# Performance work log

Measured on AMD Instinct MI355X. Metric: run time of the kernel, lower is better.

## Reference

```python
import jax, jax.numpy as jnp
import numpy as np


def _hfreq_mask(c, scale):
    # zeros over the centered (shifted) low-frequency band, ones elsewhere
    m = np.ones((c,), dtype=np.complex64)
    m[c // 2 - c // scale: c // 2 + c // scale] = 0
    return jnp.asarray(m).reshape(1, 1, 1, c)


def setup_inputs() -> dict:
    key = jax.random.key(0)
    x = jax.random.normal(key, (32, 38, 38, 728), dtype=jnp.float32)
    return {"x": x, "scale": 4}


def reference(x, scale):
    c = x.shape[-1]
    norm = jnp.asarray(np.sqrt(c), dtype=jnp.complex64)
    X = jnp.fft.fft(x.astype(jnp.complex64), axis=-1) / norm
    X = jnp.fft.fftshift(X, axes=-1)
    X = X * _hfreq_mask(c, scale)
    X = jnp.fft.ifftshift(X, axes=-1)
    y = jnp.fft.ifft(X, axis=-1) * norm
    y = jnp.real(y).astype(jnp.float32)
    return jax.nn.relu(y)
```

## Files before the change

### kernel.cpp

```cpp
#include <hip/hip_runtime.h>
#include <hip/hip_bf16.h>

#define CC 728
#define KB 736
#define NPAD 768
#define M_ROWS 46208
#define KT 23
#define NWG 2166

typedef __attribute__((ext_vector_type(8))) short bf16x8;
typedef __attribute__((ext_vector_type(8))) unsigned short ushort8;
typedef __attribute__((ext_vector_type(4))) float f32x4;

__device__ __forceinline__ unsigned short f2bf(float f) {
    unsigned int u = __float_as_uint(f);
    unsigned int r = u + 0x7fffu + ((u >> 16) & 1u);
    return (unsigned short)(r >> 16);
}

__device__ __forceinline__ void gload_lds16(const void* g, void* l) {
    __builtin_amdgcn_global_load_lds(
        (const __attribute__((address_space(1))) void*)g,
        (__attribute__((address_space(3))) void*)l,
        16, 0, 0);
}

__global__ void build_bt(unsigned short* __restrict__ bt) {
    int idx = blockIdx.x * blockDim.x + threadIdx.x;
    if (idx >= NPAD * KB) return;
    int n = idx / KB, k = idx % KB;
    float v = 0.f;
    if (n < CC && k < CC) {
        int d = n - k; if (d < 0) d += CC;
        if (d == 0) v = 0.5f;
        else if (d & 1) {
            float t = (float)(3.14159265358979323846 * (double)d / (double)CC);
            float s = ((d >> 1) & 1) ? 1.f : -1.f;
            v = s * cosf(t) / ((float)CC * sinf(t));
        }
    }
    bt[idx] = f2bf(v);
}

__global__ __launch_bounds__(256) void gemm_relu(
        const float* __restrict__ x,
        const unsigned short* __restrict__ bt,
        float* __restrict__ out) {
    __shared__ unsigned short ldsA[128 * 32];
    __shared__ unsigned short ldsB[128 * 32];

    const int tid  = threadIdx.x;
    const int lane = tid & 63;
    const int wid  = tid >> 6;
    const int wr   = wid >> 1, wc = wid & 1;
    const int l15  = lane & 15, lhi = lane >> 4;

    const int NX = 8;
    int orig  = blockIdx.x;
    int q = NWG / NX, r = NWG % NX;
    int xcd = orig % NX, local = orig / NX;
    int wgid = (xcd < r ? xcd * (q + 1) : r * (q + 1) + (xcd - r) * q) + local;
    const int bm = (wgid / 6) * 128;
    const int bn = (wgid % 6) * 128;

    f32x4 acc[4][4];
#pragma unroll
    for (int i = 0; i < 4; ++i)
#pragma unroll
        for (int j = 0; j < 4; ++j)
#pragma unroll
            for (int rr = 0; rr < 4; ++rr) acc[i][j][rr] = 0.f;

    const int arow = tid >> 2;
    const int ac   = tid & 3;

    for (int kt = 0; kt < KT; ++kt) {
        const int k0 = kt * 32;

#pragma unroll
        for (int i = 0; i < 2; ++i) {
            int rr   = i * 64 + arow;
            int gsrc = (ac - (rr >> 1)) & 3;
            gload_lds16(bt + (size_t)(bn + rr) * KB + k0 + gsrc * 8,
                        &ldsB[(i * 256 + tid) * 8]);
        }

        float4 va0[2], va1[2];
        const bool full = (k0 + 32 <= CC);
#pragma unroll
        for (int i = 0; i < 2; ++i) {
            const float* src = x + (size_t)(bm + i * 64 + arow) * CC + k0 + ac * 8;
            if (full) {
                va0[i] = ((const float4*)src)[0];
                va1[i] = ((const float4*)src)[1];
            } else {
                int cb = k0 + ac * 8;
                va0[i] = (cb     < CC) ? ((const float4*)src)[0] : make_float4(0.f,0.f,0.f,0.f);
                va1[i] = (cb + 4 < CC) ? ((const float4*)src)[1] : make_float4(0.f,0.f,0.f,0.f);
            }
        }

#pragma unroll
        for (int i = 0; i < 2; ++i) {
            int rr = i * 64 + arow;
            int sc = (ac + (rr >> 1)) & 3;
            ushort8 o;
            o[0] = f2bf(va0[i].x); o[1] = f2bf(va0[i].y);
            o[2] = f2bf(va0[i].z); o[3] = f2bf(va0[i].w);
            o[4] = f2bf(va1[i].x); o[5] = f2bf(va1[i].y);
            o[6] = f2bf(va1[i].z); o[7] = f2bf(va1[i].w);
            *(ushort8*)&ldsA[(rr * 4 + sc) * 8] = o;
        }
        __syncthreads();

        bf16x8 a[4], b[4];
#pragma unroll
        for (int mi = 0; mi < 4; ++mi) {
            int row = wr * 64 + mi * 16 + l15;
            int c   = (lhi + (row >> 1)) & 3;
            a[mi] = *(const bf16x8*)&ldsA[(row * 4 + c) * 8];
        }
#pragma unroll
        for (int nj = 0; nj < 4; ++nj) {
            int row = wc * 64 + nj * 16 + l15;
            int c   = (lhi + (row >> 1)) & 3;
            b[nj] = *(const bf16x8*)&ldsB[(row * 4 + c) * 8];
        }
#pragma unroll
        for (int mi = 0; mi < 4; ++mi)
#pragma unroll
            for (int nj = 0; nj < 4; ++nj)
                acc[mi][nj] = __builtin_amdgcn_mfma_f32_16x16x32_bf16(
                    a[mi], b[nj], acc[mi][nj], 0, 0, 0);
        __syncthreads();
    }

#pragma unroll
    for (int mi = 0; mi < 4; ++mi) {
#pragma unroll
        for (int nj = 0; nj < 4; ++nj) {
            int colg = bn + wc * 64 + nj * 16 + l15;
            if (colg < CC) {
#pragma unroll
                for (int rr = 0; rr < 4; ++rr) {
                    int rowg = bm + wr * 64 + mi * 16 + lhi * 4 + rr;
                    float v = acc[mi][nj][rr];
                    out[(size_t)rowg * CC + colg] = v > 0.f ? v : 0.f;
                }
            }
        }
    }
}

extern "C" void kernel_launch(void* const* d_in, const int* in_sizes, int n_in,
                              void* d_out, int out_size, void* d_ws, size_t ws_size,
                              hipStream_t stream) {
    const float* x = (const float*)d_in[0];
    float* out = (float*)d_out;

    unsigned short* bt = (unsigned short*)d_ws;

    build_bt<<<(NPAD * KB + 255) / 256, 256, 0, stream>>>(bt);
    gemm_relu<<<NWG, 256, 0, stream>>>(x, bt, out);
}
```

Measured before the change: 118.7 us.

## Exploit even/odd structure of circulant filter to halve GEMM work

The circulant filter matrix only couples even output indices to odd inputs (plus a 0.5 diagonal), so the 728x728 GEMM is split into two 364x364 circulant blocks. Even/odd input columns are deinterleaved into separate LDS tiles and multiplied against two smaller B matrices, while the diagonal 0.5*x term is added exactly in fp32 in the epilogue. This roughly halves the MFMA count and B traffic, and keeps the diagonal term out of bf16 rounding. In exchange, each block holds twice the accumulators, which raises register pressure, and the epilogue re-reads x.

Measured after the change: 160.7 us. +35.4%, slower.

```diff
diff --git a/kernel.cpp b/kernel.cpp
--- a/kernel.cpp
+++ b/kernel.cpp
@@ -2,11 +2,11 @@
 #include <hip/hip_bf16.h>
 
 #define CC 728
-#define KB 736
-#define NPAD 768
+#define PP 364
+#define KP 384
 #define M_ROWS 46208
-#define KT 23
-#define NWG 2166
+#define KT 12
+#define NWG 1083
 
 typedef __attribute__((ext_vector_type(8))) short bf16x8;
 typedef __attribute__((ext_vector_type(8))) unsigned short ushort8;
@@ -25,29 +25,34 @@
         16, 0, 0);
 }
 
-__global__ void build_bt(unsigned short* __restrict__ bt) {
+__global__ void build_bt(unsigned short* __restrict__ bt1,
+                         unsigned short* __restrict__ bt2) {
     int idx = blockIdx.x * blockDim.x + threadIdx.x;
-    if (idx >= NPAD * KB) return;
-    int n = idx / KB, k = idx % KB;
+    if (idx >= 2 * KP * KP) return;
+    int mat = idx / (KP * KP);
+    int rem = idx % (KP * KP);
+    int n = rem / KP, k = rem % KP;
     float v = 0.f;
-    if (n < CC && k < CC) {
-        int d = n - k; if (d < 0) d += CC;
-        if (d == 0) v = 0.5f;
-        else if (d & 1) {
-            float t = (float)(3.14159265358979323846 * (double)d / (double)CC);
-            float s = ((d >> 1) & 1) ? 1.f : -1.f;
-            v = s * cosf(t) / ((float)CC * sinf(t));
-        }
+    if (n < PP && k < PP) {
+        int m = n - k - (mat == 0 ? 1 : 0);
+        if (m < 0) m += PP;
+        int d = 2 * m + 1;
+        float t = (float)(3.14159265358979323846 * (double)d / (double)CC);
+        float s = ((d >> 1) & 1) ? 1.f : -1.f;
+        v = s * cosf(t) / ((float)CC * sinf(t));
     }
-    bt[idx] = f2bf(v);
+    (mat == 0 ? bt1 : bt2)[n * KP + k] = f2bf(v);
 }
 
 __global__ __launch_bounds__(256) void gemm_relu(
         const float* __restrict__ x,
-        const unsigned short* __restrict__ bt,
+        const unsigned short* __restrict__ bt1,
+        const unsigned short* __restrict__ bt2,
         float* __restrict__ out) {
-    __shared__ unsigned short ldsA[128 * 32];
-    __shared__ unsigned short ldsB[128 * 32];
+    __shared__ unsigned short ldsE[128 * 32];
+    __shared__ unsigned short ldsO[128 * 32];
+    __shared__ unsigned short ldsB1[128 * 32];
+    __shared__ unsigned short ldsB2[128 * 32];
 
     const int tid  = threadIdx.x;
     const int lane = tid & 63;
@@ -56,82 +61,94 @@
     const int l15  = lane & 15, lhi = lane >> 4;
 
     const int NX = 8;
-    int orig  = blockIdx.x;
+    int orig = blockIdx.x;
     int q = NWG / NX, r = NWG % NX;
     int xcd = orig % NX, local = orig / NX;
     int wgid = (xcd < r ? xcd * (q + 1) : r * (q + 1) + (xcd - r) * q) + local;
-    const int bm = (wgid / 6) * 128;
-    const int bn = (wgid % 6) * 128;
+    const int bm  = (wgid / 3) * 128;
+    const int bnp = (wgid % 3) * 128;
 
-    f32x4 acc[4][4];
+    f32x4 acc_e[4][4], acc_o[4][4];
 #pragma unroll
     for (int i = 0; i < 4; ++i)
 #pragma unroll
         for (int j = 0; j < 4; ++j)
 #pragma unroll
-            for (int rr = 0; rr < 4; ++rr) acc[i][j][rr] = 0.f;
+            for (int rr = 0; rr < 4; ++rr) { acc_e[i][j][rr] = 0.f; acc_o[i][j][rr] = 0.f; }
 
-    const int arow = tid >> 2;
-    const int ac   = tid & 3;
+    const int arow = tid >> 1;
+    const int ah   = tid & 1;
+    const int brow = tid >> 2;
+    const int bc   = tid & 3;
 
     for (int kt = 0; kt < KT; ++kt) {
         const int k0 = kt * 32;
 
 #pragma unroll
         for (int i = 0; i < 2; ++i) {
-            int rr   = i * 64 + arow;
-            int gsrc = (ac - (rr >> 1)) & 3;
-            gload_lds16(bt + (size_t)(bn + rr) * KB + k0 + gsrc * 8,
-                        &ldsB[(i * 256 + tid) * 8]);
+            int rr   = i * 64 + brow;
+            int gsrc = (bc - (rr >> 1)) & 3;
+            size_t srcoff = (size_t)(bnp + rr) * KP + k0 + gsrc * 8;
+            gload_lds16(bt1 + srcoff, &ldsB1[(i * 256 + tid) * 8]);
+            gload_lds16(bt2 + srcoff, &ldsB2[(i * 256 + tid) * 8]);
         }
 
-        float4 va0[2], va1[2];
-        const bool full = (k0 + 32 <= CC);
+        float4 va[8];
+        const int cb0 = 2 * k0 + ah * 32;
+        const float* srcA = x + (size_t)(bm + arow) * CC + cb0;
+        const bool full = (cb0 + 32 <= CC);
+        if (full) {
 #pragma unroll
-        for (int i = 0; i < 2; ++i) {
-            const float* src = x + (size_t)(bm + i * 64 + arow) * CC + k0 + ac * 8;
-            if (full) {
-                va0[i] = ((const float4*)src)[0];
-                va1[i] = ((const float4*)src)[1];
-            } else {
-                int cb = k0 + ac * 8;
-                va0[i] = (cb     < CC) ? ((const float4*)src)[0] : make_float4(0.f,0.f,0.f,0.f);
-                va1[i] = (cb + 4 < CC) ? ((const float4*)src)[1] : make_float4(0.f,0.f,0.f,0.f);
-            }
+            for (int i = 0; i < 8; ++i) va[i] = ((const float4*)srcA)[i];
+        } else {
+#pragma unroll
+            for (int i = 0; i < 8; ++i)
+                va[i] = (cb0 + 4 * i < CC) ? ((const float4*)srcA)[i]
+                                           : make_float4(0.f, 0.f, 0.f, 0.f);
         }
 
+        {
+            int rot = (arow >> 1) & 3;
 #pragma unroll
-        for (int i = 0; i < 2; ++i) {
-            int rr = i * 64 + arow;
-            int sc = (ac + (rr >> 1)) & 3;
-            ushort8 o;
-            o[0] = f2bf(va0[i].x); o[1] = f2bf(va0[i].y);
-            o[2] = f2bf(va0[i].z); o[3] = f2bf(va0[i].w);
-            o[4] = f2bf(va1[i].x); o[5] = f2bf(va1[i].y);
-            o[6] = f2bf(va1[i].z); o[7] = f2bf(va1[i].w);
-            *(ushort8*)&ldsA[(rr * 4 + sc) * 8] = o;
+            for (int c = 0; c < 2; ++c) {
+                ushort8 oe, oo;
+#pragma unroll
+                for (int p = 0; p < 4; ++p) {
+                    float4 f = va[c * 4 + p];
+                    oe[2 * p]     = f2bf(f.x); oo[2 * p]     = f2bf(f.y);
+                    oe[2 * p + 1] = f2bf(f.z); oo[2 * p + 1] = f2bf(f.w);
+                }
+                int sc = ((ah * 2 + c) + rot) & 3;
+                *(ushort8*)&ldsE[(arow * 4 + sc) * 8] = oe;
+                *(ushort8*)&ldsO[(arow * 4 + sc) * 8] = oo;
+            }
         }
         __syncthreads();
 
-        bf16x8 a[4], b[4];
+        bf16x8 aE[4], aO[4], b1[4], b2[4];
 #pragma unroll
         for (int mi = 0; mi < 4; ++mi) {
             int row = wr * 64 + mi * 16 + l15;
             int c   = (lhi + (row >> 1)) & 3;
-            a[mi] = *(const bf16x8*)&ldsA[(row * 4 + c) * 8];
+            aE[mi] = *(const bf16x8*)&ldsE[(row * 4 + c) * 8];
+            aO[mi] = *(const bf16x8*)&ldsO[(row * 4 + c) * 8];
         }
 #pragma unroll
         for (int nj = 0; nj < 4; ++nj) {
             int row = wc * 64 + nj * 16 + l15;
             int c   = (lhi + (row >> 1)) & 3;
-            b[nj] = *(const bf16x8*)&ldsB[(row * 4 + c) * 8];
+            b1[nj] = *(const bf16x8*)&ldsB1[(row * 4 + c) * 8];
+            b2[nj] = *(const bf16x8*)&ldsB2[(row * 4 + c) * 8];
         }
 #pragma unroll
         for (int mi = 0; mi < 4; ++mi)
 #pragma unroll
-            for (int nj = 0; nj < 4; ++nj)
-                acc[mi][nj] = __builtin_amdgcn_mfma_f32_16x16x32_bf16(
-                    a[mi], b[nj], acc[mi][nj], 0, 0, 0);
+            for (int nj = 0; nj < 4; ++nj) {
+                acc_e[mi][nj] = __builtin_amdgcn_mfma_f32_16x16x32_bf16(
+                    aO[mi], b1[nj], acc_e[mi][nj], 0, 0, 0);
+                acc_o[mi][nj] = __builtin_amdgcn_mfma_f32_16x16x32_bf16(
+                    aE[mi], b2[nj], acc_o[mi][nj], 0, 0, 0);
+            }
         __syncthreads();
     }
 
@@ -139,13 +156,19 @@
     for (int mi = 0; mi < 4; ++mi) {
 #pragma unroll
         for (int nj = 0; nj < 4; ++nj) {
-            int colg = bn + wc * 64 + nj * 16 + l15;
-            if (colg < CC) {
+            int colp = bnp + wc * 64 + nj * 16 + l15;
+            if (colp < PP) {
 #pragma unroll
                 for (int rr = 0; rr < 4; ++rr) {
                     int rowg = bm + wr * 64 + mi * 16 + lhi * 4 + rr;
-                    float v = acc[mi][nj][rr];
-                    out[(size_t)rowg * CC + colg] = v > 0.f ? v : 0.f;
+                    size_t base = (size_t)rowg * CC + 2 * colp;
+                    float2 xv = *(const float2*)&x[base];
+                    float2 o;
+                    float ye = 0.5f * xv.x + acc_e[mi][nj][rr];
+                    float yo = 0.5f * xv.y + acc_o[mi][nj][rr];
+                    o.x = ye > 0.f ? ye : 0.f;
+                    o.y = yo > 0.f ? yo : 0.f;
+                    *(float2*)&out[base] = o;
                 }
             }
         }
@@ -158,8 +181,9 @@
     const float* x = (const float*)d_in[0];
     float* out = (float*)d_out;
 
-    unsigned short* bt = (unsigned short*)d_ws;
+    unsigned short* bt1 = (unsigned short*)d_ws;
+    unsigned short* bt2 = bt1 + KP * KP;
 
-    build_bt<<<(NPAD * KB + 255) / 256, 256, 0, stream>>>(bt);
-    gemm_relu<<<NWG, 256, 0, stream>>>(x, bt, out);
+    build_bt<<<(2 * KP * KP + 255) / 256, 256, 0, stream>>>(bt1, bt2);
+    gemm_relu<<<NWG, 256, 0, stream>>>(x, bt1, bt2, out);
 }
```
